# Kernel optimization log

Hardware: AMD Instinct MI355X
Metric: run time of the kernel (lower is better)

The kernel has to match this reference:

```python
import jax, jax.numpy as jnp
import numpy as np

ENC_H = 512      # encoder_hidden_dim -> encoder_out feature = 2*ENC_H
DEC_H = 512      # decoder_hidden_dim
B, S = 32, 2048  # batch, max_seq_len


def setup_inputs() -> dict:
    key = jax.random.key(0)
    k1, k2, k3, k4, k5, k6, k7 = jax.random.split(key, 7)
    encoder_out = jax.random.normal(k1, (B, S, 2 * ENC_H), dtype=jnp.float32)
    hidden = jax.random.normal(k2, (B, DEC_H), dtype=jnp.float32)
    lengths = jax.random.randint(k3, (B,), 1, S + 1, dtype=jnp.int64)
    in_dim = 2 * ENC_H + DEC_H
    # torch nn.Linear default init scale
    attn_w = jax.random.uniform(k4, (DEC_H, in_dim), jnp.float32, -1.0, 1.0) / np.sqrt(in_dim)
    attn_b = jax.random.uniform(k5, (DEC_H,), jnp.float32, -1.0, 1.0) / np.sqrt(in_dim)
    v_w = jax.random.uniform(k6, (1, DEC_H), jnp.float32, -1.0, 1.0) / np.sqrt(DEC_H)
    v_b = jax.random.uniform(k7, (1,), jnp.float32, -1.0, 1.0) / np.sqrt(DEC_H)
    return {"encoder_out": encoder_out, "hidden": hidden, "lengths": lengths,
            "attn_w": attn_w, "attn_b": attn_b, "v_w": v_w, "v_b": v_b}


def reference(encoder_out, hidden, lengths, attn_w, attn_b, v_w, v_b):
    # encoder_out: [B,S,2E], hidden: [B,D], lengths: [B]
    Bc, Sc, _ = encoder_out.shape
    h = jnp.broadcast_to(hidden[:, None, :], (Bc, Sc, hidden.shape[-1]))
    temp = jnp.concatenate([h, encoder_out], axis=2)           # [B,S,D+2E]
    e = jnp.tanh(jnp.einsum('bsf,df->bsd', temp, attn_w) + attn_b)  # [B,S,D]
    scores = jnp.einsum('bsd,d->bs', e, v_w[0]) + v_b[0]       # [B,S]
    mask = jnp.arange(Sc)[None, :] < lengths[:, None]          # [B,S]
    scores = jnp.where(mask, scores, -jnp.inf)
    energy = jax.nn.softmax(scores, axis=1)                    # softmax over valid positions
    energy = jnp.where(mask, energy, 0.0)                      # padded positions stay exactly 0
    context = jnp.einsum('bs,bse->be', energy, encoder_out)    # [B,2E]
    return context
```

## Files before the change

kernel.cpp:

```cpp
#include <hip/hip_runtime.h>
#include <hip/hip_bf16.h>
#include <math.h>

typedef __attribute__((ext_vector_type(4))) short short4v;
typedef __attribute__((ext_vector_type(8))) short short8;
typedef __attribute__((ext_vector_type(16))) float f32x16;

static constexpr int B  = 32;
static constexpr int S  = 2048;
static constexpr int D  = 512;
static constexpr int KE = 1024;
static constexpr int IN = 1536;

__device__ __forceinline__ unsigned pk2(float lo, float hi) {
    __hip_bfloat162 t = __float22bfloat162_rn(make_float2(lo, hi));
    unsigned u;
    __builtin_memcpy(&u, &t, 4);
    return u;
}

__device__ __forceinline__ short4v pack4(float4 f) {
    unsigned u2[2] = { pk2(f.x, f.y), pk2(f.z, f.w) };
    short4v r;
    __builtin_memcpy(&r, u2, 8);
    return r;
}

__device__ __forceinline__ short8 pack8(float4 f0, float4 f1) {
    unsigned u[4] = { pk2(f0.x, f0.y), pk2(f0.z, f0.w), pk2(f1.x, f1.y), pk2(f1.z, f1.w) };
    short8 r;
    __builtin_memcpy(&r, u, 16);
    return r;
}

__device__ __forceinline__ short8 cat44(short4v lo, short4v hi) {
    short8 r;
    __builtin_memcpy(&r, &lo, 8);
    __builtin_memcpy(((char*)&r) + 8, &hi, 8);
    return r;
}

__device__ __forceinline__ float tanh_fast(float x) {
    float e = __expf(2.0f * x);
    return (e - 1.0f) * __builtin_amdgcn_rcpf(e + 1.0f);
}

__global__ void k_prep(const float* __restrict__ attn_w,
                       const float* __restrict__ hidden,
                       const float* __restrict__ attn_b,
                       unsigned short* __restrict__ Bf,
                       float* __restrict__ u) {
    if (blockIdx.x < 256) {
        int o = blockIdx.x * 256 + threadIdx.x;
        int l6  = o & 63;
        int grp = o >> 6;
        int d = (grp & 15) * 32 + (l6 & 31);
        int k = (grp >> 4) * 16 + (l6 >> 5) * 8;
        const float* src = attn_w + (size_t)d * IN + 512 + k;
        float4 f0 = *(const float4*)src;
        float4 f1 = *(const float4*)(src + 4);
        ((short8*)Bf)[o] = pack8(f0, f1);
    } else {
        int gid = (blockIdx.x - 256) * 256 + threadIdx.x;
        int b = gid >> 9;
        int d = gid & (D - 1);
        const float* h = hidden + b * D;
        const float* w = attn_w + (size_t)d * IN;
        float acc = attn_b[d];
        for (int k = 0; k < D; k += 4) {
            float4 hv = *(const float4*)(h + k);
            float4 wv = *(const float4*)(w + k);
            acc += hv.x * wv.x + hv.y * wv.y + hv.z * wv.z + hv.w * wv.w;
        }
        u[gid] = acc;
    }
}

#define LOADB(K, DST) do {                                     \
    _Pragma("unroll")                                          \
    for (int _jt = 0; _jt < 4; _jt++)                          \
        DST[_jt] = bb[(size_t)(K) * 1024 + _jt * 64];          \
} while (0)

__global__ __launch_bounds__(256, 3) void k_scores(
    const float* __restrict__ enc, const unsigned short* __restrict__ Bfrag,
    const float* __restrict__ u, const float* __restrict__ v_w,
    const float* __restrict__ v_b, const int* __restrict__ lengths,
    float* __restrict__ scores)
{
    __shared__ short4v ldsA[2][32 * 19];
    __shared__ float sPart[4][32];

    const int b   = blockIdx.y;
    const int s0  = blockIdx.x * 32;
    const int len = lengths[b];
    if (s0 >= len) return;

    const int tid = threadIdx.x;
    const int w   = tid >> 6;
    const int l   = tid & 63;

    const float* encb = enc + ((size_t)b * S + s0) * KE;
    const int mr = tid >> 4;
    const int cw = tid & 15;
    const float* aG = encb + (size_t)mr * KE + cw * 4;
    const int wbase = mr * 19 + cw;

    const short8* bb = (const short8*)Bfrag + (w * 4) * 64 + l;

    f32x16 acc[4];
    #pragma unroll
    for (int jt = 0; jt < 4; jt++)
        #pragma unroll
        for (int e = 0; e < 16; e++) acc[jt][e] = 0.f;

    short8 pb[2][4];
    LOADB(0, pb[0]);
    LOADB(1, pb[1]);

    {
        float4 g0 = *(const float4*)aG;
        float4 g1 = *(const float4*)(aG + (size_t)16 * KE);
        ldsA[0][wbase]           = pack4(g0);
        ldsA[0][wbase + 16 * 19] = pack4(g1);
    }
    __syncthreads();

    const int rb0 = (l & 31) * 19 + (l >> 5) * 2;

    #pragma unroll 1
    for (int c = 0; c < 16; ++c) {
        const int buf = c & 1;
        const int cn  = (c + 1) & 15;
        float4 g0 = *(const float4*)(aG + cn * 64);
        float4 g1 = *(const float4*)(aG + (size_t)16 * KE + cn * 64);
        #pragma unroll
        for (int t2 = 0; t2 < 4; ++t2) {
            const short4v* base = &ldsA[buf][t2 * 4];
            short8 a0 = cat44(base[rb0], base[rb0 + 1]);
            const int bp = t2 & 1;
            #pragma unroll
            for (int jt = 0; jt < 4; jt++)
                acc[jt] = __builtin_amdgcn_mfma_f32_32x32x16_bf16(a0, pb[bp][jt], acc[jt], 0, 0, 0);
            LOADB((c * 4 + t2 + 2) & 63, pb[bp]);
        }
        __syncthreads();
        ldsA[buf ^ 1][wbase]           = pack4(g0);
        ldsA[buf ^ 1][wbase + 16 * 19] = pack4(g1);
        __syncthreads();
    }

    float vv[4], uu[4];
    const float* ub = u + b * D;
    #pragma unroll
    for (int jt = 0; jt < 4; jt++) {
        int d = w * 128 + jt * 32 + (l & 31);
        vv[jt] = v_w[d];
        uu[jt] = ub[d];
    }
    float red[16];
    #pragma unroll
    for (int r = 0; r < 16; r++) {
        float s = 0.f;
        #pragma unroll
        for (int jt = 0; jt < 4; jt++)
            s += vv[jt] * tanh_fast(acc[jt][r] + uu[jt]);
        red[r] = s;
    }
    #pragma unroll
    for (int off = 16; off >= 1; off >>= 1)
        #pragma unroll
        for (int r = 0; r < 16; r++)
            red[r] += __shfl_xor(red[r], off);
    if ((l & 31) == 0) {
        int hb = (l >> 5) * 4;
        #pragma unroll
        for (int r = 0; r < 16; r++)
            sPart[w][(r & 3) + 8 * (r >> 2) + hb] = red[r];
    }
    __syncthreads();
    if (tid < 32)
        scores[b * S + s0 + tid] =
            sPart[0][tid] + sPart[1][tid] + sPart[2][tid] + sPart[3][tid] + v_b[0];
}

__global__ void k_softmax(const float* __restrict__ scores,
                          const int* __restrict__ lengths,
                          float* __restrict__ energy) {
    const int b = blockIdx.x;
    const int len = lengths[b];
    const int tid = threadIdx.x;
    const int lane = tid & 63, wave = tid >> 6;
    __shared__ float red[4];
    const float* sc = scores + b * S;

    float m = -INFINITY;
    for (int s = tid; s < len; s += 256) m = fmaxf(m, sc[s]);
    #pragma unroll
    for (int off = 32; off >= 1; off >>= 1) m = fmaxf(m, __shfl_xor(m, off));
    if (lane == 0) red[wave] = m;
    __syncthreads();
    m = fmaxf(fmaxf(red[0], red[1]), fmaxf(red[2], red[3]));
    __syncthreads();

    float sum = 0.f;
    for (int s = tid; s < len; s += 256) sum += __expf(sc[s] - m);
    #pragma unroll
    for (int off = 32; off >= 1; off >>= 1) sum += __shfl_xor(sum, off);
    if (lane == 0) red[wave] = sum;
    __syncthreads();
    float inv = 1.f / (red[0] + red[1] + red[2] + red[3]);

    for (int s = tid; s < len; s += 256) energy[b * S + s] = __expf(sc[s] - m) * inv;
}

__global__ void k_context(const float* __restrict__ enc,
                          const float* __restrict__ energy,
                          const int* __restrict__ lengths,
                          float* __restrict__ out) {
    const int b = blockIdx.y;
    const int len = lengths[b];
    const int s0 = blockIdx.x * 128;
    if (s0 >= len) return;
    const int s1 = min(s0 + 128, len);
    const int tid = threadIdx.x;
    const float4* encb = (const float4*)(enc + (size_t)b * S * KE);
    const float* en = energy + b * S;
    float4 acc[8];
    #pragma unroll
    for (int i = 0; i < 8; i++) acc[i] = make_float4(0.f, 0.f, 0.f, 0.f);
    int s = s0;
    for (; s + 8 <= s1; s += 8) {
        #pragma unroll
        for (int i = 0; i < 8; i++) {
            float wgt = en[s + i];
            float4 v = encb[(size_t)(s + i) * 256 + tid];
            acc[i].x += wgt * v.x; acc[i].y += wgt * v.y;
            acc[i].z += wgt * v.z; acc[i].w += wgt * v.w;
        }
    }
    for (; s < s1; s++) {
        float wgt = en[s];
        float4 v = encb[(size_t)s * 256 + tid];
        acc[0].x += wgt * v.x; acc[0].y += wgt * v.y;
        acc[0].z += wgt * v.z; acc[0].w += wgt * v.w;
    }
    #pragma unroll
    for (int i = 1; i < 8; i++) {
        acc[0].x += acc[i].x; acc[0].y += acc[i].y;
        acc[0].z += acc[i].z; acc[0].w += acc[i].w;
    }
    float* o = out + b * KE + tid * 4;
    atomicAdd(o + 0, acc[0].x);
    atomicAdd(o + 1, acc[0].y);
    atomicAdd(o + 2, acc[0].z);
    atomicAdd(o + 3, acc[0].w);
}

extern "C" void kernel_launch(void* const* d_in, const int* in_sizes, int n_in,
                              void* d_out, int out_size, void* d_ws, size_t ws_size,
                              hipStream_t stream) {
    const float* enc    = (const float*)d_in[0];
    const float* hidden = (const float*)d_in[1];
    const int*   lengths= (const int*)d_in[2];
    const float* attn_w = (const float*)d_in[3];
    const float* attn_b = (const float*)d_in[4];
    const float* v_w    = (const float*)d_in[5];
    const float* v_b    = (const float*)d_in[6];
    float* out = (float*)d_out;

    float* ws     = (float*)d_ws;
    float* u      = ws;
    float* scores = u + B * D;
    float* energy = scores + B * S;
    unsigned short* Bf = (unsigned short*)(energy + B * S);

    (void)hipMemsetAsync(d_out, 0, (size_t)out_size * sizeof(float), stream);
    k_prep  <<<dim3(320), 256, 0, stream>>>(attn_w, hidden, attn_b, Bf, u);
    k_scores<<<dim3(S / 32, B), 256, 0, stream>>>(enc, Bf, u, v_w, v_b, lengths, scores);
    k_softmax<<<dim3(B), 256, 0, stream>>>(scores, lengths, energy);
    k_context<<<dim3(16, B), 256, 0, stream>>>(enc, energy, lengths, out);
}
```

Measured before the change: 468.0 us.

## Fuse softmax and context into score kernel with unnormalized exp accumulation

Merges the separate softmax and context kernels into the score kernel. Each 32-row tile computes exp(score) without subtracting the row max, atomically adds the exp sum to a per-batch denominator, and accumulates exp-weighted encoder rows into a numerator buffer. A small normalize kernel then divides the numerator by the denominator. This drops the second full read of encoder_out and two launches, since the rows are likely still cached after the score pass. The cost is more atomics per block and a risk of exp overflow because the max is not subtracted; with scores bounded by the tanh and v_w sizes this is probably safe.

```diff
diff --git a/kernel.cpp b/kernel.cpp
--- a/kernel.cpp
+++ b/kernel.cpp
@@ -82,14 +82,15 @@
         DST[_jt] = bb[(size_t)(K) * 1024 + _jt * 64];          \
 } while (0)
 
-__global__ __launch_bounds__(256, 3) void k_scores(
+__global__ __launch_bounds__(256, 3) void k_fused(
     const float* __restrict__ enc, const unsigned short* __restrict__ Bfrag,
     const float* __restrict__ u, const float* __restrict__ v_w,
     const float* __restrict__ v_b, const int* __restrict__ lengths,
-    float* __restrict__ scores)
+    float* __restrict__ num, float* __restrict__ den)
 {
     __shared__ short4v ldsA[2][32 * 19];
     __shared__ float sPart[4][32];
+    __shared__ float sExp[32];
 
     const int b   = blockIdx.y;
     const int s0  = blockIdx.x * 32;
@@ -179,82 +180,52 @@
             sPart[w][(r & 3) + 8 * (r >> 2) + hb] = red[r];
     }
     __syncthreads();
-    if (tid < 32)
-        scores[b * S + s0 + tid] =
-            sPart[0][tid] + sPart[1][tid] + sPart[2][tid] + sPart[3][tid] + v_b[0];
-}
-
-__global__ void k_softmax(const float* __restrict__ scores,
-                          const int* __restrict__ lengths,
-                          float* __restrict__ energy) {
-    const int b = blockIdx.x;
-    const int len = lengths[b];
-    const int tid = threadIdx.x;
-    const int lane = tid & 63, wave = tid >> 6;
-    __shared__ float red[4];
-    const float* sc = scores + b * S;
-
-    float m = -INFINITY;
-    for (int s = tid; s < len; s += 256) m = fmaxf(m, sc[s]);
-    #pragma unroll
-    for (int off = 32; off >= 1; off >>= 1) m = fmaxf(m, __shfl_xor(m, off));
-    if (lane == 0) red[wave] = m;
+
+    if (tid < 32) {
+        float sc = sPart[0][tid] + sPart[1][tid] + sPart[2][tid] + sPart[3][tid] + v_b[0];
+        float wexp = (s0 + tid < len) ? __expf(sc) : 0.f;
+        sExp[tid] = wexp;
+        float dsum = wexp;
+        #pragma unroll
+        for (int off = 16; off >= 1; off >>= 1) dsum += __shfl_xor(dsum, off);
+        if (tid == 0) atomicAdd(den + b, dsum);
+    }
     __syncthreads();
-    m = fmaxf(fmaxf(red[0], red[1]), fmaxf(red[2], red[3]));
-    __syncthreads();
-
-    float sum = 0.f;
-    for (int s = tid; s < len; s += 256) sum += __expf(sc[s] - m);
-    #pragma unroll
-    for (int off = 32; off >= 1; off >>= 1) sum += __shfl_xor(sum, off);
-    if (lane == 0) red[wave] = sum;
-    __syncthreads();
-    float inv = 1.f / (red[0] + red[1] + red[2] + red[3]);
-
-    for (int s = tid; s < len; s += 256) energy[b * S + s] = __expf(sc[s] - m) * inv;
-}
-
-__global__ void k_context(const float* __restrict__ enc,
-                          const float* __restrict__ energy,
-                          const int* __restrict__ lengths,
-                          float* __restrict__ out) {
-    const int b = blockIdx.y;
-    const int len = lengths[b];
-    const int s0 = blockIdx.x * 128;
-    if (s0 >= len) return;
-    const int s1 = min(s0 + 128, len);
-    const int tid = threadIdx.x;
-    const float4* encb = (const float4*)(enc + (size_t)b * S * KE);
-    const float* en = energy + b * S;
-    float4 acc[8];
-    #pragma unroll
-    for (int i = 0; i < 8; i++) acc[i] = make_float4(0.f, 0.f, 0.f, 0.f);
-    int s = s0;
-    for (; s + 8 <= s1; s += 8) {
-        #pragma unroll
-        for (int i = 0; i < 8; i++) {
-            float wgt = en[s + i];
-            float4 v = encb[(size_t)(s + i) * 256 + tid];
-            acc[i].x += wgt * v.x; acc[i].y += wgt * v.y;
-            acc[i].z += wgt * v.z; acc[i].w += wgt * v.w;
+
+    const float4* e4 = (const float4*)encb;
+    float4 cacc[4];
+    #pragma unroll
+    for (int j = 0; j < 4; j++) cacc[j] = make_float4(0.f, 0.f, 0.f, 0.f);
+    #pragma unroll
+    for (int i = 0; i < 8; i++) {
+        #pragma unroll
+        for (int j = 0; j < 4; j++) {
+            float wgt = sExp[i * 4 + j];
+            float4 v = e4[(size_t)(i * 4 + j) * 256 + tid];
+            cacc[j].x += wgt * v.x; cacc[j].y += wgt * v.y;
+            cacc[j].z += wgt * v.z; cacc[j].w += wgt * v.w;
         }
     }
-    for (; s < s1; s++) {
-        float wgt = en[s];
-        float4 v = encb[(size_t)s * 256 + tid];
-        acc[0].x += wgt * v.x; acc[0].y += wgt * v.y;
-        acc[0].z += wgt * v.z; acc[0].w += wgt * v.w;
-    }
-    #pragma unroll
-    for (int i = 1; i < 8; i++) {
-        acc[0].x += acc[i].x; acc[0].y += acc[i].y;
-        acc[0].z += acc[i].z; acc[0].w += acc[i].w;
-    }
-    float* o = out + b * KE + tid * 4;
-    atomicAdd(o + 0, acc[0].x);
-    atomicAdd(o + 1, acc[0].y);
-    atomicAdd(o + 2, acc[0].z);
-    atomicAdd(o + 3, acc[0].w);
+    #pragma unroll
+    for (int j = 1; j < 4; j++) {
+        cacc[0].x += cacc[j].x; cacc[0].y += cacc[j].y;
+        cacc[0].z += cacc[j].z; cacc[0].w += cacc[j].w;
+    }
+    float* o = num + b * KE + tid * 4;
+    atomicAdd(o + 0, cacc[0].x);
+    atomicAdd(o + 1, cacc[0].y);
+    atomicAdd(o + 2, cacc[0].z);
+    atomicAdd(o + 3, cacc[0].w);
+}
+
+__global__ void k_norm(const float* __restrict__ num, const float* __restrict__ den,
+                       float* __restrict__ out) {
+    int b = blockIdx.x;
+    int t = threadIdx.x;
+    float inv = 1.f / den[b];
+    float4 v = ((const float4*)(num + b * KE))[t];
+    v.x *= inv; v.y *= inv; v.z *= inv; v.w *= inv;
+    ((float4*)(out + b * KE))[t] = v;
 }
 
 extern "C" void kernel_launch(void* const* d_in, const int* in_sizes, int n_in,
@@ -269,15 +240,14 @@
     const float* v_b    = (const float*)d_in[6];
     float* out = (float*)d_out;
 
-    float* ws     = (float*)d_ws;
-    float* u      = ws;
-    float* scores = u + B * D;
-    float* energy = scores + B * S;
-    unsigned short* Bf = (unsigned short*)(energy + B * S);
-
-    (void)hipMemsetAsync(d_out, 0, (size_t)out_size * sizeof(float), stream);
-    k_prep  <<<dim3(320), 256, 0, stream>>>(attn_w, hidden, attn_b, Bf, u);
-    k_scores<<<dim3(S / 32, B), 256, 0, stream>>>(enc, Bf, u, v_w, v_b, lengths, scores);
-    k_softmax<<<dim3(B), 256, 0, stream>>>(scores, lengths, energy);
-    k_context<<<dim3(16, B), 256, 0, stream>>>(enc, energy, lengths, out);
-}
+    float* ws  = (float*)d_ws;
+    float* u   = ws;
+    float* num = u + B * D;
+    float* den = num + B * KE;
+    unsigned short* Bf = (unsigned short*)(den + 32);
+
+    (void)hipMemsetAsync(num, 0, (size_t)(B * KE + B) * sizeof(float), stream);
+    k_prep <<<dim3(320), 256, 0, stream>>>(attn_w, hidden, attn_b, Bf, u);
+    k_fused<<<dim3(S / 32, B), 256, 0, stream>>>(enc, Bf, u, v_w, v_b, lengths, num, den);
+    k_norm <<<dim3(B), 256, 0, stream>>>(num, den, out);
+}
```

Result: faster. 451.8 us (-3.5%).
